# Kernel tuning notes

Measured on AMD Instinct MI355X. Metric: run time of the kernel, lower is better.

## Reference

```python
import math
import jax, jax.numpy as jnp
import numpy as np

B, K, D, N = 64, 16384, 128, 500000
T = 0.07          # nce_t
MOM = 0.5         # nce_momentum (EMA for memory bank update)


def setup_inputs() -> dict:
    key = jax.random.key(0)
    k0, k1, k2, k3, k4, k5 = jax.random.split(key, 6)
    stdv = 1.0 / math.sqrt(D / 3.0)
    memory_l = jax.random.uniform(k0, (N, D), dtype=jnp.float32) * (2 * stdv) - stdv
    memory_ab = jax.random.uniform(k1, (N, D), dtype=jnp.float32) * (2 * stdv) - stdv
    l = jax.random.normal(k2, (B, D), dtype=jnp.float32)
    ab = jax.random.normal(k3, (B, D), dtype=jnp.float32)
    # unique positive indices so the index_copy_ scatter is well-defined
    y = jax.random.permutation(k4, N)[:B].astype(jnp.int64)
    idx = jax.random.randint(k5, (B, K + 1), 0, N, dtype=jnp.int64)
    idx = idx.at[:, 0].set(y)  # slot 0 holds the positive sample, as in torch code
    return {"l": l, "ab": ab, "memory_l": memory_l, "memory_ab": memory_ab,
            "y": y, "idx": idx}


def reference(l, ab, memory_l, memory_ab, y, idx):
    # gather -> batched dot-product scoring (use_softmax=True branch: just /T)
    weight_l = memory_l[idx]            # (B, K+1, D)  gather from bank
    out_ab = jnp.einsum('bkd,bd->bk', weight_l, ab)[..., None] / T   # (B, K+1, 1)
    weight_ab = memory_ab[idx]          # (B, K+1, D)
    out_l = jnp.einsum('bkd,bd->bk', weight_ab, l)[..., None] / T    # (B, K+1, 1)

    # momentum EMA + L2-normalize + scatter update of the memory banks (no-grad in torch)
    def ema_update(mem, feat):
        pos = mem[y] * MOM + feat * (1.0 - MOM)                       # (B, D)
        pos = pos / jnp.sqrt(jnp.sum(pos * pos, axis=1, keepdims=True))
        return mem.at[y].set(pos)

    new_memory_l = ema_update(memory_l, l)
    new_memory_ab = ema_update(memory_ab, ab)
    return out_l, out_ab, new_memory_l, new_memory_ab
```

## Files before the change

### kernel.cpp

```cpp
#include <hip/hip_runtime.h>
#include <math.h>

#define B_    64
#define KP1   16385
#define D_    128
#define N_    500000
#define INV_T (1.0f / 0.07f)
#define MOM_  0.5f

#define NBLK   2048
#define NTHR   (NBLK * 256)
#define NGRP   (NBLK * 8)
#define BK_    (B_ * KP1)
#define TOT_   (2 * BK_)
#define NE4B   (N_ * D_ / 4)
#define CPITER 31
#define BASEQ  32
#define REMG   32

__device__ __forceinline__ float dot4(const float4 r, const float4 f) {
    return r.x * f.x + r.y * f.y + r.z * f.z + r.w * f.w;
}

__device__ __forceinline__ void score_quad(
        unsigned t, int glane,
        const float* __restrict__ l, const float* __restrict__ ab,
        const float* __restrict__ mem_l, const float* __restrict__ mem_ab,
        const int* __restrict__ idx, float* __restrict__ out) {
    const unsigned bank0 = (t >= (unsigned)BK_) ? 1u : 0u;
    const unsigned u0    = t - bank0 * (unsigned)BK_;
    const unsigned b0    = u0 / KP1;
    const unsigned k0    = u0 - b0 * KP1;

    if (k0 <= (unsigned)(KP1 - 4)) {
        const float* mem  = bank0 ? mem_l : mem_ab;
        const float* feat = bank0 ? ab    : l;
        const float4 f = ((const float4*)(feat + (size_t)b0 * D_))[glane];

        const int i0 = idx[u0],     i1 = idx[u0 + 1];
        const int i2 = idx[u0 + 2], i3 = idx[u0 + 3];
        const float4 r0 = ((const float4*)(mem + (size_t)i0 * D_))[glane];
        const float4 r1 = ((const float4*)(mem + (size_t)i1 * D_))[glane];
        const float4 r2 = ((const float4*)(mem + (size_t)i2 * D_))[glane];
        const float4 r3 = ((const float4*)(mem + (size_t)i3 * D_))[glane];

        float v0 = dot4(r0, f), v1 = dot4(r1, f);
        float v2 = dot4(r2, f), v3 = dot4(r3, f);
        #pragma unroll
        for (int m = 16; m >= 1; m >>= 1) {
            v0 += __shfl_xor(v0, m);
            v1 += __shfl_xor(v1, m);
            v2 += __shfl_xor(v2, m);
            v3 += __shfl_xor(v3, m);
        }
        float vv = glane == 1 ? v1 : glane == 2 ? v2 : glane == 3 ? v3 : v0;
        if (glane < 4) out[t + glane] = vv * INV_T;
    } else {
        #pragma unroll
        for (int i = 0; i < 4; ++i) {
            const unsigned ti = t + i;
            const unsigned bk = (ti >= (unsigned)BK_) ? 1u : 0u;
            const unsigned u  = ti - bk * (unsigned)BK_;
            const unsigned b  = u / KP1;
            const float* mem  = bk ? mem_l : mem_ab;
            const float* feat = bk ? ab    : l;
            const float4 f = ((const float4*)(feat + (size_t)b * D_))[glane];
            const int ri = idx[u];
            const float4 r = ((const float4*)(mem + (size_t)ri * D_))[glane];
            float v = dot4(r, f);
            #pragma unroll
            for (int m = 16; m >= 1; m >>= 1) v += __shfl_xor(v, m);
            if (glane == 0) out[ti] = v * INV_T;
        }
    }
}

__global__ __launch_bounds__(256)
void fused_kernel(const float* __restrict__ l,
                  const float* __restrict__ ab,
                  const float* __restrict__ mem_l,
                  const float* __restrict__ mem_ab,
                  const int* __restrict__ idx,
                  float* __restrict__ out,
                  float* __restrict__ out_mem_l) {
    const unsigned tid   = blockIdx.x * 256u + threadIdx.x;
    const int      glane = threadIdx.x & 31;
    const unsigned g     = (blockIdx.x << 3) + (threadIdx.x >> 5);

    const float4* srcL  = (const float4*)mem_l;
    const float4* srcAB = (const float4*)mem_ab;
    float4* dstL  = (float4*)out_mem_l;
    float4* dstAB = dstL + NE4B;

    for (int j = 0; j < BASEQ; ++j) {
        if (j < CPITER) {
            const size_t e = (size_t)j * NTHR + tid;
            if (e < (size_t)NE4B) {
                dstL[e]  = srcL[e];
                dstAB[e] = srcAB[e];
            }
        }
        score_quad(4u * (g + (unsigned)j * NGRP), glane,
                   l, ab, mem_l, mem_ab, idx, out);
    }
    if (g < REMG)
        score_quad(4u * ((unsigned)BASEQ * NGRP + g), glane,
                   l, ab, mem_l, mem_ab, idx, out);
}

__global__ __launch_bounds__(128)
void ema_update_kernel(const float* __restrict__ l,
                       const float* __restrict__ ab,
                       const float* __restrict__ mem_l,
                       const float* __restrict__ mem_ab,
                       const int* __restrict__ y,
                       float* __restrict__ out_mem_l,
                       float* __restrict__ out_mem_ab) {
    const int b    = blockIdx.x;
    const int wave = threadIdx.x >> 6;
    const int lane = threadIdx.x & 63;
    const int yb   = y[b];

    const float* mem  = wave ? mem_ab     : mem_l;
    const float* feat = wave ? ab         : l;
    float*       om   = wave ? out_mem_ab : out_mem_l;

    const float2 m2 = ((const float2*)(mem  + (size_t)yb * D_))[lane];
    const float2 f2 = ((const float2*)(feat + (size_t)b  * D_))[lane];

    float px = m2.x * MOM_ + f2.x * (1.0f - MOM_);
    float py = m2.y * MOM_ + f2.y * (1.0f - MOM_);
    float ss = px * px + py * py;
    #pragma unroll
    for (int m = 32; m >= 1; m >>= 1) ss += __shfl_xor(ss, m);
    const float rn = 1.0f / sqrtf(ss);

    ((float2*)(om + (size_t)yb * D_))[lane] = make_float2(px * rn, py * rn);
}

extern "C" void kernel_launch(void* const* d_in, const int* in_sizes, int n_in,
                              void* d_out, int out_size, void* d_ws, size_t ws_size,
                              hipStream_t stream) {
    const float* l      = (const float*)d_in[0];
    const float* ab     = (const float*)d_in[1];
    const float* mem_l  = (const float*)d_in[2];
    const float* mem_ab = (const float*)d_in[3];
    const int*   y      = (const int*)d_in[4];
    const int*   idx    = (const int*)d_in[5];
    float* out = (float*)d_out;

    float* out_mem_l  = out + (size_t)TOT_;
    float* out_mem_ab = out_mem_l + (size_t)N_ * D_;

    fused_kernel<<<NBLK, 256, 0, stream>>>(l, ab, mem_l, mem_ab, idx,
                                           out, out_mem_l);
    ema_update_kernel<<<B_, 128, 0, stream>>>(l, ab, mem_l, mem_ab, y,
                                              out_mem_l, out_mem_ab);
}
```

Measured before the change: 327.8 us.

## Score one quad per thread serially and run bank copy after scoring

Switches the scoring work split from 32 lanes cooperating on each group of four gathered rows with shuffle reductions to one thread computing four full 128-element dot products by itself. Indices are loaded as an int4 and results stored as a float4. The memory-bank copy moves out of the interleaved loop into a separate pass after scoring. This removes shuffle reductions and idle lanes, but each thread now walks whole rows, so the gather loads across a wavefront are no longer coalesced. Copy and gather traffic also overlap less.

Result: slower. 1.215 ms (+270.5%).

```diff
diff --git a/kernel.cpp b/kernel.cpp
--- a/kernel.cpp
+++ b/kernel.cpp
@@ -4,73 +4,69 @@
 #define B_    64
 #define KP1   16385
 #define D_    128
-#define N_    500000
+#define NROW  500000
 #define INV_T (1.0f / 0.07f)
 #define MOM_  0.5f
 
+#define BK_    (B_ * KP1)
+#define TOT_   (2 * BK_)
+#define NQUAD  (TOT_ / 4)
+#define NE4B   (NROW * (D_ / 4))
 #define NBLK   2048
 #define NTHR   (NBLK * 256)
-#define NGRP   (NBLK * 8)
-#define BK_    (B_ * KP1)
-#define TOT_   (2 * BK_)
-#define NE4B   (N_ * D_ / 4)
-#define CPITER 31
-#define BASEQ  32
-#define REMG   32
+#define REMQ   (NQUAD - NTHR)
+#define CP_FULL (NE4B / NTHR)
 
 __device__ __forceinline__ float dot4(const float4 r, const float4 f) {
     return r.x * f.x + r.y * f.y + r.z * f.z + r.w * f.w;
 }
 
 __device__ __forceinline__ void score_quad(
-        unsigned t, int glane,
+        unsigned q,
         const float* __restrict__ l, const float* __restrict__ ab,
         const float* __restrict__ mem_l, const float* __restrict__ mem_ab,
         const int* __restrict__ idx, float* __restrict__ out) {
-    const unsigned bank0 = (t >= (unsigned)BK_) ? 1u : 0u;
-    const unsigned u0    = t - bank0 * (unsigned)BK_;
-    const unsigned b0    = u0 / KP1;
-    const unsigned k0    = u0 - b0 * KP1;
+    const unsigned u0   = 4u * q;
+    const unsigned bank = (u0 >= (unsigned)BK_) ? 1u : 0u;
+    const unsigned uu   = u0 - bank * (unsigned)BK_;
+    const unsigned b    = uu / KP1;
+    const unsigned k0   = uu - b * KP1;
+
+    const float* mem  = bank ? mem_l : mem_ab;
+    const float* feat = bank ? ab    : l;
 
     if (k0 <= (unsigned)(KP1 - 4)) {
-        const float* mem  = bank0 ? mem_l : mem_ab;
-        const float* feat = bank0 ? ab    : l;
-        const float4 f = ((const float4*)(feat + (size_t)b0 * D_))[glane];
+        const int4 i4 = *(const int4*)(idx + uu);
+        const float4* r0 = (const float4*)(mem + (size_t)i4.x * D_);
+        const float4* r1 = (const float4*)(mem + (size_t)i4.y * D_);
+        const float4* r2 = (const float4*)(mem + (size_t)i4.z * D_);
+        const float4* r3 = (const float4*)(mem + (size_t)i4.w * D_);
+        const float4* fp = (const float4*)(feat + (size_t)b * D_);
 
-        const int i0 = idx[u0],     i1 = idx[u0 + 1];
-        const int i2 = idx[u0 + 2], i3 = idx[u0 + 3];
-        const float4 r0 = ((const float4*)(mem + (size_t)i0 * D_))[glane];
-        const float4 r1 = ((const float4*)(mem + (size_t)i1 * D_))[glane];
-        const float4 r2 = ((const float4*)(mem + (size_t)i2 * D_))[glane];
-        const float4 r3 = ((const float4*)(mem + (size_t)i3 * D_))[glane];
-
-        float v0 = dot4(r0, f), v1 = dot4(r1, f);
-        float v2 = dot4(r2, f), v3 = dot4(r3, f);
-        #pragma unroll
-        for (int m = 16; m >= 1; m >>= 1) {
-            v0 += __shfl_xor(v0, m);
-            v1 += __shfl_xor(v1, m);
-            v2 += __shfl_xor(v2, m);
-            v3 += __shfl_xor(v3, m);
+        float a0 = 0.f, a1 = 0.f, a2 = 0.f, a3 = 0.f;
+        #pragma unroll 4
+        for (int j = 0; j < 32; ++j) {
+            const float4 f = fp[j];
+            a0 += dot4(r0[j], f);
+            a1 += dot4(r1[j], f);
+            a2 += dot4(r2[j], f);
+            a3 += dot4(r3[j], f);
         }
-        float vv = glane == 1 ? v1 : glane == 2 ? v2 : glane == 3 ? v3 : v0;
-        if (glane < 4) out[t + glane] = vv * INV_T;
+        float4 o;
+        o.x = a0 * INV_T; o.y = a1 * INV_T; o.z = a2 * INV_T; o.w = a3 * INV_T;
+        *(float4*)(out + u0) = o;
     } else {
         #pragma unroll
         for (int i = 0; i < 4; ++i) {
-            const unsigned ti = t + i;
-            const unsigned bk = (ti >= (unsigned)BK_) ? 1u : 0u;
-            const unsigned u  = ti - bk * (unsigned)BK_;
-            const unsigned b  = u / KP1;
-            const float* mem  = bk ? mem_l : mem_ab;
-            const float* feat = bk ? ab    : l;
-            const float4 f = ((const float4*)(feat + (size_t)b * D_))[glane];
-            const int ri = idx[u];
-            const float4 r = ((const float4*)(mem + (size_t)ri * D_))[glane];
-            float v = dot4(r, f);
-            #pragma unroll
-            for (int m = 16; m >= 1; m >>= 1) v += __shfl_xor(v, m);
-            if (glane == 0) out[ti] = v * INV_T;
+            const unsigned u  = u0 + i;
+            const unsigned ub = u - bank * (unsigned)BK_;
+            const unsigned bi = ub / KP1;
+            const float4* rp = (const float4*)(mem + (size_t)idx[ub] * D_);
+            const float4* fp = (const float4*)(feat + (size_t)bi * D_);
+            float a = 0.f;
+            #pragma unroll 4
+            for (int j = 0; j < 32; ++j) a += dot4(rp[j], fp[j]);
+            out[u] = a * INV_T;
         }
     }
 }
@@ -82,30 +78,30 @@
                   const float* __restrict__ mem_ab,
                   const int* __restrict__ idx,
                   float* __restrict__ out,
-                  float* __restrict__ out_mem_l) {
-    const unsigned tid   = blockIdx.x * 256u + threadIdx.x;
-    const int      glane = threadIdx.x & 31;
-    const unsigned g     = (blockIdx.x << 3) + (threadIdx.x >> 5);
+                  float* __restrict__ out_mem_l,
+                  float* __restrict__ out_mem_ab) {
+    const unsigned tid = blockIdx.x * 256u + threadIdx.x;
 
-    const float4* srcL  = (const float4*)mem_l;
-    const float4* srcAB = (const float4*)mem_ab;
-    float4* dstL  = (float4*)out_mem_l;
-    float4* dstAB = dstL + NE4B;
+    score_quad(tid, l, ab, mem_l, mem_ab, idx, out);
+    if (tid < REMQ)
+        score_quad((unsigned)NTHR + tid, l, ab, mem_l, mem_ab, idx, out);
 
-    for (int j = 0; j < BASEQ; ++j) {
-        if (j < CPITER) {
-            const size_t e = (size_t)j * NTHR + tid;
-            if (e < (size_t)NE4B) {
-                dstL[e]  = srcL[e];
-                dstAB[e] = srcAB[e];
-            }
-        }
-        score_quad(4u * (g + (unsigned)j * NGRP), glane,
-                   l, ab, mem_l, mem_ab, idx, out);
+    const float4* srcL = (const float4*)mem_l;
+    const float4* srcA = (const float4*)mem_ab;
+    float4* dstL = (float4*)out_mem_l;
+    float4* dstA = (float4*)out_mem_ab;
+
+    #pragma unroll 2
+    for (int j = 0; j < CP_FULL; ++j) {
+        const size_t e = (size_t)j * NTHR + tid;
+        dstL[e] = srcL[e];
+        dstA[e] = srcA[e];
     }
-    if (g < REMG)
-        score_quad(4u * ((unsigned)BASEQ * NGRP + g), glane,
-                   l, ab, mem_l, mem_ab, idx, out);
+    const size_t e = (size_t)CP_FULL * NTHR + tid;
+    if (e < (size_t)NE4B) {
+        dstL[e] = srcL[e];
+        dstA[e] = srcA[e];
+    }
 }
 
 __global__ __launch_bounds__(128)
@@ -150,10 +146,10 @@
     float* out = (float*)d_out;
 
     float* out_mem_l  = out + (size_t)TOT_;
-    float* out_mem_ab = out_mem_l + (size_t)N_ * D_;
+    float* out_mem_ab = out_mem_l + (size_t)NROW * D_;
 
     fused_kernel<<<NBLK, 256, 0, stream>>>(l, ab, mem_l, mem_ab, idx,
-                                           out, out_mem_l);
+                                           out, out_mem_l, out_mem_ab);
     ema_update_kernel<<<B_, 128, 0, stream>>>(l, ab, mem_l, mem_ab, y,
                                               out_mem_l, out_mem_ab);
 }
```
